# Performance work log

Hardware: AMD Instinct MI355X
Metric: run time of the kernel (lower is better)

## Reference

```python
import jax, jax.numpy as jnp
import numpy as np
from jax import lax

B, CI, CO, H, W = 32, 64, 64, 128, 128
NUM_EXPERTS = 5
NUM_TASKS = 10  # num_tasks=9 + 1 internal global task
K = 5


def setup_inputs() -> dict:
    key = jax.random.key(0)
    ks = jax.random.split(key, 9)
    # kaiming_uniform_ with a=sqrt(5), fan_out -> bound = sqrt(6/((1+5)*fan_out))
    def kaiming(k, co, ci, ksz):
        fan_out = co * ksz * ksz
        bound = np.sqrt(6.0 / (6.0 * fan_out))
        return jax.random.uniform(k, (co, ci, ksz, ksz), jnp.float32, -bound, bound)
    gw_bound = 1.0 / np.sqrt(NUM_TASKS)
    return {
        "x": jax.random.normal(ks[0], (B, CI, H, W), jnp.float32),
        "task_id": jax.random.randint(ks[1], (B,), 0, NUM_TASKS),
        "gate_w": jax.random.uniform(ks[2], (NUM_EXPERTS * CO, NUM_TASKS), jnp.float32, -gw_bound, gw_bound),
        "gate_b": jax.random.uniform(ks[3], (NUM_EXPERTS * CO,), jnp.float32, -gw_bound, gw_bound),
        "w5": kaiming(ks[4], CO, CI, 5),
        "w3": kaiming(ks[5], CO, CI, 3),
        "w1": kaiming(ks[6], CO, CI, 1),
        "wavg3": kaiming(ks[7], CO, CI, 1),
        "wavg5": kaiming(ks[8], CO, CI, 1),
    }


def _expert_bank(w5, w3, w1, wavg3, wavg5):
    # All experts expressed as 5x5 kernels, stacked: [E, O, I, 5, 5]
    pad = lambda w, p: jnp.pad(w, ((0, 0), (0, 0), (p, p), (p, p)))
    avg3 = jnp.full((3, 3), 1.0 / 9.0, w5.dtype)
    avg5 = jnp.full((5, 5), 1.0 / 25.0, w5.dtype)
    e_conv5 = w5
    e_conv3 = pad(w3, 1)
    e_conv1 = pad(w1, 2)
    e_avg3 = pad(wavg3 * avg3[None, None], 1)  # [O,I,1,1]*[3,3] broadcast
    e_avg5 = wavg5 * avg5[None, None]
    return jnp.stack([e_conv5, e_conv3, e_conv1, e_avg3, e_avg5])


def reference(x, task_id, gate_w, gate_b, w5, w3, w1, wavg3, wavg5):
    # Gate: one-hot task -> per-(expert, out_channel) routing weights
    t = jax.nn.one_hot(task_id, NUM_TASKS, dtype=x.dtype)          # [B, T]
    g = t @ gate_w.T + gate_b                                       # [B, E*O]
    g = jax.nn.softmax(g.reshape(-1, NUM_EXPERTS, CO), axis=1)      # [B, E, O]

    experts = _expert_bank(w5, w3, w1, wavg3, wavg5)                # [E, O, I, 5, 5]
    # Batched kernel synthesis (replaces per-sample python loop of einsums)
    w = jnp.einsum('eoikl,beo->boikl', experts, g)                  # [B, O, I, 5, 5]

    # Per-sample conv2d, stride 1, 'same' padding
    def conv1(xi, wi):
        return lax.conv_general_dilated(
            xi[None], wi, (1, 1), 'SAME',
            dimension_numbers=('NCHW', 'OIHW', 'NCHW'))[0]
    y = jax.vmap(conv1)(x, w)                                       # [B, O, H, W]
    # conv_type='final' -> Identity subsequent layer; eval mode -> task_id unchanged
    return y, task_id
```

## Files before the change

kernel.cpp:

```cpp
#include <hip/hip_runtime.h>

#define WK_OFFSET_BYTES 71368704ull

using bf16x8   = __attribute__((ext_vector_type(8)))  __bf16;
using floatx16 = __attribute__((ext_vector_type(16))) float;

static __device__ __forceinline__ unsigned short f2bf(float f) {
    unsigned int u = __float_as_uint(f);
    u += 0x7FFFu + ((u >> 16) & 1u);
    return (unsigned short)(u >> 16);
}

static __device__ __forceinline__ floatx16 mfma16(bf16x8 a, bf16x8 b, floatx16 c) {
    return __builtin_amdgcn_mfma_f32_32x32x16_bf16(a, b, c, 0, 0, 0);
}

static __device__ __forceinline__ void gload_lds16(const void* g, void* l) {
    __builtin_amdgcn_global_load_lds(
        (const __attribute__((address_space(1))) void*)g,
        (__attribute__((address_space(3))) void*)l, 16, 0, 0);
}

__global__ __launch_bounds__(256) void pre_kernel(
    const float* __restrict__ x,
    const float* __restrict__ gate_w, const float* __restrict__ gate_b,
    const float* __restrict__ w5, const float* __restrict__ w3,
    const float* __restrict__ w1, const float* __restrict__ wavg3,
    const float* __restrict__ wavg5, const int* __restrict__ task_id,
    unsigned short* __restrict__ xt, unsigned short* __restrict__ wk,
    float* __restrict__ out_task)
{
    const int blk = blockIdx.x;
    const int tid = threadIdx.x;
    __shared__ float g[5][64];

    if (blk < 4224) {
        const int b  = blk / 132;
        const int hp = blk - b * 132;
        const int h  = hp - 2;
        const bool vrow = (h >= 0) && (h < 128);
        unsigned short* dst_row = xt + (size_t)blk * 8448;

        for (int i = tid; i < 1056; i += 256) {
            int cc = i / 132;
            int wp = i - cc * 132;
            unsigned int pk[4] = {0u, 0u, 0u, 0u};
            if (vrow && wp >= 2 && wp < 130) {
                const float* xp = x + (((size_t)(b * 64 + cc * 8) * 128 + h) * 128 + (wp - 2));
                #pragma unroll
                for (int j = 0; j < 4; ++j) {
                    unsigned short lo = f2bf(xp[(2 * j)     * 16384]);
                    unsigned short hi = f2bf(xp[(2 * j + 1) * 16384]);
                    pk[j] = (unsigned int)lo | ((unsigned int)hi << 16);
                }
            }
            *(uint4*)(dst_row + (size_t)i * 8) = make_uint4(pk[0], pk[1], pk[2], pk[3]);
        }
    } else {
        const int pb = blk - 4224;
        const int t = pb >> 4;
        const int chunk = pb & 15;

        if (tid < 64) {
            float l[5];
            float m = -1e30f;
            #pragma unroll
            for (int e = 0; e < 5; ++e) {
                l[e] = gate_w[(e * 64 + tid) * 10 + t] + gate_b[e * 64 + tid];
                m = fmaxf(m, l[e]);
            }
            float s = 0.f;
            #pragma unroll
            for (int e = 0; e < 5; ++e) { l[e] = expf(l[e] - m); s += l[e]; }
            float inv = 1.f / s;
            #pragma unroll
            for (int e = 0; e < 5; ++e) g[e][tid] = l[e] * inv;
        }
        __syncthreads();

        for (int it = 0; it < 25; ++it) {
            int idx = chunk * 6400 + it * 256 + tid;
            int ci  = idx & 63;
            int o   = (idx >> 6) & 63;
            int tap = idx >> 12;
            int ky = tap / 5, kx = tap - ky * 5;

            float v = g[0][o] * w5[(o * 64 + ci) * 25 + tap];
            bool in3 = (ky >= 1 && ky <= 3 && kx >= 1 && kx <= 3);
            if (in3) {
                v += g[1][o] * w3[(o * 64 + ci) * 9 + (ky - 1) * 3 + (kx - 1)];
                v += g[3][o] * wavg3[o * 64 + ci] * (1.f / 9.f);
            }
            if (ky == 2 && kx == 2) v += g[2][o] * w1[o * 64 + ci];
            v += g[4][o] * wavg5[o * 64 + ci] * (1.f / 25.f);

            wk[(t * 25 + tap) * 4096 + o * 64 + ci] = f2bf(v);
        }

        if (pb == 0 && tid < 32) out_task[tid] = (float)task_id[tid];
    }
}

__global__ __launch_bounds__(256, 2) void conv_kernel(
    const unsigned short* __restrict__ xt, const unsigned short* __restrict__ wk,
    const int* __restrict__ task_id, float* __restrict__ out)
{
    __shared__ unsigned short ibuf[2][16896];

    const int blk = ((blockIdx.x & 7) << 7) | (blockIdx.x >> 3);
    const int b  = blk >> 5;
    const int ht = blk & 31;
    const int t  = task_id[b];

    const int tid  = threadIdx.x;
    const int lane = tid & 63;
    const int wc   = tid >> 6;
    const int lane31 = lane & 31;
    const int laneh  = lane >> 5;

    floatx16 acc[4][2];
    #pragma unroll
    for (int o = 0; o < 4; ++o)
        #pragma unroll
        for (int c = 0; c < 2; ++c)
            #pragma unroll
            for (int r = 0; r < 16; ++r) acc[o][c][r] = 0.f;

    const unsigned short* wkt = wk + t * 102400;
    const size_t ibase0 = ((size_t)(b * 132 + ht * 4)) * 8448;

    auto stage_i = [&](int s, int q) {
        const unsigned short* gsrc = xt + ibase0 + q * 2112;
        unsigned short* ldst = &ibuf[s][0];
        #pragma unroll
        for (int j = 0; j < 8; ++j) {
            int i = j * 256 + tid;
            int r = i / 264;
            int rem = i - r * 264;
            gload_lds16(gsrc + (size_t)r * 8448 + rem * 8, ldst + i * 8);
        }
        if (tid < 64) {
            int i = 2048 + tid;
            int r = i / 264;
            int rem = i - r * 264;
            gload_lds16(gsrc + (size_t)r * 8448 + rem * 8, ldst + i * 8);
        }
    };

    stage_i(0, 0);
    asm volatile("s_waitcnt vmcnt(0)" ::: "memory");
    __builtin_amdgcn_s_barrier();
    __builtin_amdgcn_sched_barrier(0);

    for (int q = 0; q < 4; ++q) {
        const int s = q & 1;
        if (q < 3) stage_i(s ^ 1, q + 1);

        const unsigned short* ib = &ibuf[s][0];
        const unsigned short* wq = wkt + q * 16 + laneh * 8;
        __builtin_amdgcn_s_setprio(1);
        #pragma unroll
        for (int kx = 0; kx < 5; ++kx) {
            bf16x8 aF[5][2];
            #pragma unroll
            for (int ky = 0; ky < 5; ++ky) {
                const unsigned short* ap = wq + (ky * 5 + kx) * 4096 + lane31 * 64;
                aF[ky][0] = *(const bf16x8*)(ap);
                aF[ky][1] = *(const bf16x8*)(ap + 2048);
            }
            #pragma unroll
            for (int hr = 0; hr < 8; ++hr) {
                bf16x8 bb = *(const bf16x8*)(ib + hr * 2112 + laneh * 1056
                                             + (wc * 32 + lane31 + kx) * 8);
                #pragma unroll
                for (int ky = 0; ky < 5; ++ky) {
                    const int o = hr - ky;
                    if (o >= 0 && o < 4) {
                        acc[o][0] = mfma16(aF[ky][0], bb, acc[o][0]);
                        acc[o][1] = mfma16(aF[ky][1], bb, acc[o][1]);
                    }
                }
            }
        }
        __builtin_amdgcn_s_setprio(0);

        if (q < 3) {
            asm volatile("s_waitcnt vmcnt(0) lgkmcnt(0)" ::: "memory");
            __builtin_amdgcn_s_barrier();
            __builtin_amdgcn_sched_barrier(0);
        }
    }

    #pragma unroll
    for (int o = 0; o < 4; ++o) {
        const int h = ht * 4 + o;
        #pragma unroll
        for (int c = 0; c < 2; ++c) {
            const int w = wc * 32 + lane31;
            #pragma unroll
            for (int reg = 0; reg < 16; ++reg) {
                int co = c * 32 + (reg & 3) + 8 * (reg >> 2) + 4 * laneh;
                out[((size_t)(b * 64 + co) * 128 + h) * 128 + w] = acc[o][c][reg];
            }
        }
    }
}

extern "C" void kernel_launch(void* const* d_in, const int* in_sizes, int n_in,
                              void* d_out, int out_size, void* d_ws, size_t ws_size,
                              hipStream_t stream) {
    const float* x       = (const float*)d_in[0];
    const int*   task_id = (const int*)  d_in[1];
    const float* gate_w  = (const float*)d_in[2];
    const float* gate_b  = (const float*)d_in[3];
    const float* w5      = (const float*)d_in[4];
    const float* w3      = (const float*)d_in[5];
    const float* w1      = (const float*)d_in[6];
    const float* wavg3   = (const float*)d_in[7];
    const float* wavg5   = (const float*)d_in[8];

    float* out = (float*)d_out;
    float* out_task = out + 32 * 64 * 128 * 128;

    unsigned short* xt = (unsigned short*)d_ws;
    unsigned short* wk = (unsigned short*)((char*)d_ws + WK_OFFSET_BYTES);

    pre_kernel<<<dim3(4384), dim3(256), 0, stream>>>(
        x, gate_w, gate_b, w5, w3, w1, wavg3, wavg5, task_id, xt, wk, out_task);
    conv_kernel<<<dim3(1024), dim3(256), 0, stream>>>(xt, wk, task_id, out);
}
```

Baseline: 369.8 us.

## Retile conv blocks to 8x64 output and stage weights in LDS

```diff
diff --git a/kernel.cpp b/kernel.cpp
--- a/kernel.cpp
+++ b/kernel.cpp
@@ -105,16 +105,20 @@
     const unsigned short* __restrict__ xt, const unsigned short* __restrict__ wk,
     const int* __restrict__ task_id, float* __restrict__ out)
 {
-    __shared__ unsigned short ibuf[2][16896];
+    __shared__ __align__(16) unsigned short ibuf[13056];
+    __shared__ __align__(16) unsigned short wlds[25600];
 
     const int blk = ((blockIdx.x & 7) << 7) | (blockIdx.x >> 3);
     const int b  = blk >> 5;
-    const int ht = blk & 31;
+    const int ht = (blk >> 1) & 15;
+    const int wt = blk & 1;
     const int t  = task_id[b];
 
     const int tid  = threadIdx.x;
     const int lane = tid & 63;
-    const int wc   = tid >> 6;
+    const int wave = tid >> 6;
+    const int rg = wave >> 1;
+    const int wc = wave & 1;
     const int lane31 = lane & 31;
     const int laneh  = lane >> 5;
 
@@ -127,51 +131,60 @@
             for (int r = 0; r < 16; ++r) acc[o][c][r] = 0.f;
 
     const unsigned short* wkt = wk + t * 102400;
-    const size_t ibase0 = ((size_t)(b * 132 + ht * 4)) * 8448;
-
-    auto stage_i = [&](int s, int q) {
-        const unsigned short* gsrc = xt + ibase0 + q * 2112;
-        unsigned short* ldst = &ibuf[s][0];
-        #pragma unroll
-        for (int j = 0; j < 8; ++j) {
-            int i = j * 256 + tid;
-            int r = i / 264;
-            int rem = i - r * 264;
-            gload_lds16(gsrc + (size_t)r * 8448 + rem * 8, ldst + i * 8);
-        }
-        if (tid < 64) {
-            int i = 2048 + tid;
-            int r = i / 264;
-            int rem = i - r * 264;
-            gload_lds16(gsrc + (size_t)r * 8448 + rem * 8, ldst + i * 8);
-        }
-    };
-
-    stage_i(0, 0);
-    asm volatile("s_waitcnt vmcnt(0)" ::: "memory");
-    __builtin_amdgcn_s_barrier();
-    __builtin_amdgcn_sched_barrier(0);
+    const size_t ibase0 = ((size_t)(b * 132 + ht * 8)) * 8448;
+    const int wbase = wt * 64;
 
     for (int q = 0; q < 4; ++q) {
-        const int s = q & 1;
-        if (q < 3) stage_i(s ^ 1, q + 1);
-
-        const unsigned short* ib = &ibuf[s][0];
-        const unsigned short* wq = wkt + q * 16 + laneh * 8;
+        {
+            const unsigned short* gs = xt + ibase0 + q * 2112 + wbase * 8;
+            #pragma unroll
+            for (int j = 0; j < 7; ++j) {
+                if (j < 6 || tid < 96) {
+                    int i = j * 256 + tid;
+                    int run = i / 68;
+                    int off = i - run * 68;
+                    int r   = run >> 1;
+                    int cc  = run & 1;
+                    gload_lds16(gs + (size_t)r * 8448 + cc * 1056 + off * 8,
+                                ibuf + (size_t)i * 8);
+                }
+            }
+        }
+        {
+            const unsigned short* gs = wkt + q * 16;
+            #pragma unroll
+            for (int j = 0; j < 13; ++j) {
+                if (j < 12 || tid < 128) {
+                    int i = j * 256 + tid;
+                    int tap = i >> 7;
+                    int rem = i & 127;
+                    int cih = rem >> 6;
+                    int co  = rem & 63;
+                    gload_lds16(gs + tap * 4096 + co * 64 + cih * 8,
+                                wlds + (size_t)i * 8);
+                }
+            }
+        }
+        asm volatile("s_waitcnt vmcnt(0)" ::: "memory");
+        __builtin_amdgcn_s_barrier();
+        __builtin_amdgcn_sched_barrier(0);
+
         __builtin_amdgcn_s_setprio(1);
         #pragma unroll
         for (int kx = 0; kx < 5; ++kx) {
+            const unsigned short* wkx = wlds + kx * 1024 + laneh * 512 + lane31 * 8;
+            const unsigned short* ibb = ibuf + laneh * 544
+                                      + (wc * 32 + lane31 + kx) * 8;
             bf16x8 aF[5][2];
             #pragma unroll
             for (int ky = 0; ky < 5; ++ky) {
-                const unsigned short* ap = wq + (ky * 5 + kx) * 4096 + lane31 * 64;
+                const unsigned short* ap = wkx + ky * 5120;
                 aF[ky][0] = *(const bf16x8*)(ap);
-                aF[ky][1] = *(const bf16x8*)(ap + 2048);
+                aF[ky][1] = *(const bf16x8*)(ap + 256);
             }
             #pragma unroll
             for (int hr = 0; hr < 8; ++hr) {
-                bf16x8 bb = *(const bf16x8*)(ib + hr * 2112 + laneh * 1056
-                                             + (wc * 32 + lane31 + kx) * 8);
+                bf16x8 bb = *(const bf16x8*)(ibb + (rg * 4 + hr) * 1088);
                 #pragma unroll
                 for (int ky = 0; ky < 5; ++ky) {
                     const int o = hr - ky;
@@ -184,19 +197,17 @@
         }
         __builtin_amdgcn_s_setprio(0);
 
-        if (q < 3) {
-            asm volatile("s_waitcnt vmcnt(0) lgkmcnt(0)" ::: "memory");
-            __builtin_amdgcn_s_barrier();
-            __builtin_amdgcn_sched_barrier(0);
-        }
+        asm volatile("s_waitcnt lgkmcnt(0)" ::: "memory");
+        __builtin_amdgcn_s_barrier();
+        __builtin_amdgcn_sched_barrier(0);
     }
 
     #pragma unroll
     for (int o = 0; o < 4; ++o) {
-        const int h = ht * 4 + o;
+        const int h = ht * 8 + rg * 4 + o;
+        const int w = wbase + wc * 32 + lane31;
         #pragma unroll
         for (int c = 0; c < 2; ++c) {
-            const int w = wc * 32 + lane31;
             #pragma unroll
             for (int reg = 0; reg < 16; ++reg) {
                 int co = c * 32 + (reg & 3) + 8 * (reg >> 2) + 4 * laneh;
```

Result: faster. 343.4 us (-7.1%).
